# Performance work log

Measured on AMD Instinct MI355X. Metric: run time of the kernel, lower is better.

The kernel has to match this reference:

```python
import jax, jax.numpy as jnp
import numpy as np

N = 4096
D_IN = 3000
D_HID = 512
D_OUT = 64
NEG_SLOPE = 0.2  # LeakyReLU alpha used by GraphAttentionLayer(.., 0.2, 0.2)
MASK_FILL = -9e15


def setup_inputs() -> dict:
    key = jax.random.key(0)
    ks = jax.random.split(key, 13)

    def p(k, shape, fan_in):
        return jax.random.normal(k, shape, dtype=jnp.float32) * np.float32(1.0 / np.sqrt(fan_in))

    return {
        "features_omics1": jax.random.normal(ks[0], (N, D_IN), dtype=jnp.float32),
        "feat_adj_omics1": jax.random.randint(ks[1], (N, N), 0, 2, dtype=jnp.int32),
        "spatial_adj_omics1": jax.random.randint(ks[2], (N, N), 0, 2, dtype=jnp.int32),
        # encoder_1: GAT(D_IN -> D_HID); encoder_2: GAT(D_HID -> D_OUT)
        "W_enc1": p(ks[3], (D_IN, D_HID), D_IN),
        "a_enc1": p(ks[4], (2 * D_HID, 1), D_HID),
        "W_enc2": p(ks[5], (D_HID, D_OUT), D_HID),
        "a_enc2": p(ks[6], (2 * D_OUT, 1), D_OUT),
        # decoder_1: GAT(D_OUT -> D_HID); decoder_2: GAT(D_HID -> D_IN)
        "W_dec1": p(ks[7], (D_OUT, D_HID), D_OUT),
        "a_dec1": p(ks[8], (2 * D_HID, 1), D_HID),
        "W_dec2": p(ks[9], (D_HID, D_IN), D_HID),
        "a_dec2": p(ks[10], (2 * D_IN, 1), D_IN),
        # AttentionLayer fusion over the two views
        "w_omega": p(ks[11], (D_OUT, D_OUT), D_OUT),
        "u_omega": p(ks[12], (D_OUT, 1), D_OUT),
    }


def _gat(h, adj, W, a):
    """Canonical dense-adjacency GAT layer (pyGAT), dropout off, ELU output."""
    Wh = h @ W                                   # [N, F]
    f = W.shape[1]
    # e[i,j] = leaky_relu(a1.Wh_i + a2.Wh_j)
    e = jax.nn.leaky_relu(Wh @ a[:f] + (Wh @ a[f:]).T, NEG_SLOPE)  # [N, N]
    att = jax.nn.softmax(jnp.where(adj > 0, e, MASK_FILL), axis=1)
    return jax.nn.elu(att @ Wh)


def _encode(x, adj, W1, a1, W2, a2):
    return _gat(_gat(x, adj, W1, a1), adj, W2, a2)


def _att_fuse(e1, e2, w_omega, u_omega):
    emb = jnp.stack([e1, e2], axis=1)            # [N, 2, D]
    v = jnp.tanh(emb @ w_omega)                  # [N, 2, D]
    vu = (v @ u_omega)[..., 0]                   # [N, 2]
    alpha = jax.nn.softmax(vu + 1e-6, axis=1)    # [N, 2]
    fused = jnp.einsum('nkd,nk->nd', emb, alpha)
    return fused, alpha


def reference(features_omics1, feat_adj_omics1, spatial_adj_omics1,
              W_enc1, a_enc1, W_enc2, a_enc2,
              W_dec1, a_dec1, W_dec2, a_dec2,
              w_omega, u_omega):
    feat_emb = _encode(features_omics1, feat_adj_omics1, W_enc1, a_enc1, W_enc2, a_enc2)
    sp_emb = _encode(features_omics1, spatial_adj_omics1, W_enc1, a_enc1, W_enc2, a_enc2)
    emb_latent, alpha = _att_fuse(feat_emb, sp_emb, w_omega, u_omega)
    recon = _gat(_gat(emb_latent, spatial_adj_omics1, W_dec1, a_dec1),
                 spatial_adj_omics1, W_dec2, a_dec2)
    corr_f = _encode(recon, feat_adj_omics1, W_enc1, a_enc1, W_enc2, a_enc2)
    corr_s = _encode(recon, spatial_adj_omics1, W_enc1, a_enc1, W_enc2, a_enc2)
    corr, _ = _att_fuse(corr_f, corr_s, w_omega, u_omega)
    return emb_latent, recon, corr, alpha
```

## Files before the change

kernel.cpp:

```cpp
#include <hip/hip_runtime.h>
#include <hip/hip_bf16.h>
#include <math.h>

using u16 = unsigned short;
using u32 = unsigned int;

typedef __attribute__((ext_vector_type(8))) short s8v;
typedef __attribute__((ext_vector_type(4))) float f4v;

__device__ __forceinline__ float bf2f(u16 u) {
    u32 x = ((u32)u) << 16;
    return __builtin_bit_cast(float, x);
}
__device__ __forceinline__ u16 f2bf(float f) {
    u32 x = __builtin_bit_cast(u32, f);
    x += 0x7fffu + ((x >> 16) & 1u);
    return (u16)(x >> 16);
}

__device__ __forceinline__ f4v mfma_bf16(s8v a, s8v b, f4v c) {
    return __builtin_amdgcn_mfma_f32_16x16x32_bf16(a, b, c, 0, 0, 0);
}

#define GLL(srcp, dstp) __builtin_amdgcn_global_load_lds( \
    (const __attribute__((address_space(1))) void*)(srcp), \
    (__attribute__((address_space(3))) void*)(dstp), 16, 0, 0)

__device__ __forceinline__ void xcd_swz(int& bx, int& by, int& bz) {
    const int nx = gridDim.x, ny = gridDim.y;
    const int total = nx * ny * gridDim.z;
    int i = (bz * ny + by) * nx + bx;
    const int q = total >> 3, r = total & 7;
    const int xcd = i & 7, k = i >> 3;
    int j = ((xcd < r) ? xcd * (q + 1) : r * (q + 1) + (xcd - r) * q) + k;
    bx = j % nx; j /= nx;
    by = j % ny;
    bz = j / ny;
}

template<bool DO_ELU, bool OUT_F32>
__global__ __launch_bounds__(256) void tgemm(
    const u16* __restrict__ A, const u16* __restrict__ Bt,
    void* __restrict__ Cv, int M, int N, int K)
{
    constexpr int BM = 128, BN = 64, BK = 64;
    __shared__ __align__(16) u16 As[2][BM * BK];
    __shared__ __align__(16) u16 Bs[2][BN * BK];

    int bx = blockIdx.x, by = blockIdx.y, bz = blockIdx.z;
    xcd_swz(bx, by, bz);
    const int bm0 = by * BM, bn0 = bx * BN;
    const int tid = threadIdx.x;
    const int lane = tid & 63;
    const int wave = tid >> 6;
    const int wr = wave >> 1;
    const int wc = wave & 1;
    const int lr = lane & 15;
    const int srow = lane >> 3;
    const int schk = lane & 7;

    f4v acc[4][2] = {};

    auto stage = [&](int buf, int k0) {
#pragma unroll
        for (int ci = 0; ci < 4; ci++) {
            const int r8 = (wave * 4 + ci) * 8;
            const int row = r8 + srow;
            const int gchk = schk ^ (row & 7);
            GLL(A + (size_t)(bm0 + row) * K + k0 + gchk * 8, &As[buf][r8 * 64]);
        }
#pragma unroll
        for (int ci = 0; ci < 2; ci++) {
            const int r8 = (wave * 2 + ci) * 8;
            const int row = r8 + srow;
            int gn = bn0 + row;
            if (gn >= N) gn = N - 1;
            const int gchk = schk ^ (row & 7);
            GLL(Bt + (size_t)gn * K + k0 + gchk * 8, &Bs[buf][r8 * 64]);
        }
    };

    stage(0, 0);
    __syncthreads();
    int cur = 0;
    for (int k0 = 0; k0 < K; k0 += BK) {
        if (k0 + BK < K) stage(cur ^ 1, k0 + BK);
#pragma unroll
        for (int kk = 0; kk < 2; kk++) {
            const int cbase = (lane >> 4) + kk * 4;
            s8v a[4], b[2];
#pragma unroll
            for (int m = 0; m < 4; m++) {
                const int row = wr * 64 + m * 16 + lr;
                a[m] = *(const s8v*)&As[cur][row * 64 + (cbase ^ (row & 7)) * 8];
            }
#pragma unroll
            for (int n = 0; n < 2; n++) {
                const int row = wc * 32 + n * 16 + lr;
                b[n] = *(const s8v*)&Bs[cur][row * 64 + (cbase ^ (row & 7)) * 8];
            }
#pragma unroll
            for (int m = 0; m < 4; m++)
#pragma unroll
                for (int n = 0; n < 2; n++)
                    acc[m][n] = mfma_bf16(a[m], b[n], acc[m][n]);
        }
        __syncthreads();
        cur ^= 1;
    }

#pragma unroll
    for (int m = 0; m < 4; m++)
#pragma unroll
        for (int n = 0; n < 2; n++)
#pragma unroll
            for (int i = 0; i < 4; i++) {
                int gm = bm0 + wr * 64 + m * 16 + (lane >> 4) * 4 + i;
                int gn = bn0 + wc * 32 + n * 16 + lr;
                if (gm < M && gn < N) {
                    float val = acc[m][n][i];
                    if (DO_ELU) val = val > 0.f ? val : expm1f(val);
                    if (OUT_F32) ((float*)Cv)[(size_t)gm * N + gn] = val;
                    else         ((u16*)Cv)[(size_t)gm * N + gn] = f2bf(val);
                }
            }
}

__global__ __launch_bounds__(256) void tgemm_sk(
    const u16* __restrict__ A, const u16* __restrict__ Bt,
    float* __restrict__ P, int M, int N, int K, int KS)
{
    constexpr int BM = 128, BN = 64, BK = 64;
    __shared__ __align__(16) u16 As[2][BM * BK];
    __shared__ __align__(16) u16 Bs[2][BN * BK];

    int bx = blockIdx.x, by = blockIdx.y, kz = blockIdx.z;
    xcd_swz(bx, by, kz);
    const int bm0 = by * BM, bn0 = bx * BN;
    const int tid = threadIdx.x;
    const int lane = tid & 63;
    const int wave = tid >> 6;
    const int wr = wave >> 1;
    const int wc = wave & 1;
    const int lr = lane & 15;
    const int srow = lane >> 3;
    const int schk = lane & 7;

    f4v acc[4][2] = {};

    auto stage = [&](int buf, int k0) {
#pragma unroll
        for (int ci = 0; ci < 4; ci++) {
            const int r8 = (wave * 4 + ci) * 8;
            const int row = r8 + srow;
            const int gchk = schk ^ (row & 7);
            GLL(A + (size_t)(bm0 + row) * K + k0 + gchk * 8, &As[buf][r8 * 64]);
        }
#pragma unroll
        for (int ci = 0; ci < 2; ci++) {
            const int r8 = (wave * 2 + ci) * 8;
            const int row = r8 + srow;
            int gn = bn0 + row;
            if (gn >= N) gn = N - 1;
            const int gchk = schk ^ (row & 7);
            GLL(Bt + (size_t)gn * K + k0 + gchk * 8, &Bs[buf][r8 * 64]);
        }
    };

    const int kbeg = kz * KS, kend = kbeg + KS;
    stage(0, kbeg);
    __syncthreads();
    int cur = 0;
    for (int k0 = kbeg; k0 < kend; k0 += BK) {
        if (k0 + BK < kend) stage(cur ^ 1, k0 + BK);
#pragma unroll
        for (int kk = 0; kk < 2; kk++) {
            const int cbase = (lane >> 4) + kk * 4;
            s8v a[4], b[2];
#pragma unroll
            for (int m = 0; m < 4; m++) {
                const int row = wr * 64 + m * 16 + lr;
                a[m] = *(const s8v*)&As[cur][row * 64 + (cbase ^ (row & 7)) * 8];
            }
#pragma unroll
            for (int n = 0; n < 2; n++) {
                const int row = wc * 32 + n * 16 + lr;
                b[n] = *(const s8v*)&Bs[cur][row * 64 + (cbase ^ (row & 7)) * 8];
            }
#pragma unroll
            for (int m = 0; m < 4; m++)
#pragma unroll
                for (int n = 0; n < 2; n++)
                    acc[m][n] = mfma_bf16(a[m], b[n], acc[m][n]);
        }
        __syncthreads();
        cur ^= 1;
    }

    float* Pz = P + (size_t)kz * M * N;
#pragma unroll
    for (int m = 0; m < 4; m++)
#pragma unroll
        for (int n = 0; n < 2; n++)
#pragma unroll
            for (int i = 0; i < 4; i++) {
                int gm = bm0 + wr * 64 + m * 16 + (lane >> 4) * 4 + i;
                int gn = bn0 + wc * 32 + n * 16 + lr;
                if (gm < M && gn < N)
                    Pz[(size_t)gm * N + gn] = acc[m][n][i];
            }
}

template<bool ELU>
__global__ __launch_bounds__(256) void skred_kernel(
    const float* __restrict__ P, u16* __restrict__ out, int total, int sk)
{
    int i = blockIdx.x * 256 + threadIdx.x;
    if (i >= total) return;
    float s = 0.f;
    for (int z = 0; z < sk; z++) s += P[(size_t)z * total + i];
    if (ELU) s = s > 0.f ? s : expm1f(s);
    out[i] = f2bf(s);
}

template<bool ASP, bool SK>
__global__ __launch_bounds__(256) void tgemm2(
    const u16* __restrict__ A0, const u16* __restrict__ A1,
    const u16* __restrict__ Bt0, const u16* __restrict__ Bt1,
    void* __restrict__ Cv, int M, int N, int K, int KS)
{
    constexpr int BM = 128, BN = 64, BK = 64;
    __shared__ __align__(16) u16 As0[BM * BK];
    __shared__ __align__(16) u16 As1[ASP ? BM * BK : 8];
    __shared__ __align__(16) u16 Bs0[BN * BK];
    __shared__ __align__(16) u16 Bs1[BN * BK];

    int bx = blockIdx.x, by = blockIdx.y, kz = blockIdx.z;
    xcd_swz(bx, by, kz);
    const int bm0 = by * BM, bn0 = bx * BN;
    const int tid = threadIdx.x;
    const int lane = tid & 63;
    const int wave = tid >> 6;
    const int wr = wave >> 1;
    const int wc = wave & 1;
    const int lr = lane & 15;
    const int srow = lane >> 3;
    const int schk = lane & 7;

    f4v acc[4][2] = {};

    const int kbeg = SK ? kz * KS : 0;
    const int kend = SK ? kbeg + KS : K;
    for (int k0 = kbeg; k0 < kend; k0 += BK) {
#pragma unroll
        for (int ci = 0; ci < 4; ci++) {
            const int r8 = (wave * 4 + ci) * 8;
            const int row = r8 + srow;
            const int gchk = schk ^ (row & 7);
            const size_t goff = (size_t)(bm0 + row) * K + k0 + gchk * 8;
            GLL(A0 + goff, &As0[r8 * 64]);
            if constexpr (ASP) GLL(A1 + goff, &As1[r8 * 64]);
        }
#pragma unroll
        for (int ci = 0; ci < 2; ci++) {
            const int r8 = (wave * 2 + ci) * 8;
            const int row = r8 + srow;
            int gn = bn0 + row;
            if (gn >= N) gn = N - 1;
            const int gchk = schk ^ (row & 7);
            const size_t goff = (size_t)gn * K + k0 + gchk * 8;
            GLL(Bt0 + goff, &Bs0[r8 * 64]);
            GLL(Bt1 + goff, &Bs1[r8 * 64]);
        }
        __syncthreads();

#pragma unroll
        for (int kk = 0; kk < 2; kk++) {
            const int cbase = (lane >> 4) + kk * 4;
            s8v a0[4], a1[ASP ? 4 : 1], b0[2], b1[2];
#pragma unroll
            for (int m = 0; m < 4; m++) {
                const int row = wr * 64 + m * 16 + lr;
                const int o = row * 64 + (cbase ^ (row & 7)) * 8;
                a0[m] = *(const s8v*)&As0[o];
                if constexpr (ASP) a1[m] = *(const s8v*)&As1[o];
            }
#pragma unroll
            for (int n = 0; n < 2; n++) {
                const int row = wc * 32 + n * 16 + lr;
                const int o = row * 64 + (cbase ^ (row & 7)) * 8;
                b0[n] = *(const s8v*)&Bs0[o];
                b1[n] = *(const s8v*)&Bs1[o];
            }
#pragma unroll
            for (int m = 0; m < 4; m++)
#pragma unroll
                for (int n = 0; n < 2; n++) {
                    acc[m][n] = mfma_bf16(a0[m], b0[n], acc[m][n]);
                    acc[m][n] = mfma_bf16(a0[m], b1[n], acc[m][n]);
                    if constexpr (ASP) acc[m][n] = mfma_bf16(a1[m], b0[n], acc[m][n]);
                }
        }
        __syncthreads();
    }

#pragma unroll
    for (int m = 0; m < 4; m++)
#pragma unroll
        for (int n = 0; n < 2; n++)
#pragma unroll
            for (int i = 0; i < 4; i++) {
                int gm = bm0 + wr * 64 + m * 16 + (lane >> 4) * 4 + i;
                int gn = bn0 + wc * 32 + n * 16 + lr;
                if (gm < M && gn < N) {
                    if (SK) ((float*)Cv)[(size_t)kz * M * N + (size_t)gm * N + gn] = acc[m][n][i];
                    else    ((u16*)Cv)[(size_t)gm * N + gn] = f2bf(acc[m][n][i]);
                }
            }
}

__global__ __launch_bounds__(256) void splitA_kernel(
    const float* __restrict__ src, u16* __restrict__ hi, u16* __restrict__ lo,
    int C, int Cp)
{
    int r = blockIdx.y;
    int c = blockIdx.x * 256 + threadIdx.x;
    if (c >= Cp) return;
    float v = (c < C) ? src[(size_t)r * C + c] : 0.f;
    u16 h = f2bf(v);
    hi[(size_t)r * Cp + c] = h;
    lo[(size_t)r * Cp + c] = f2bf(v - bf2f(h));
}

__global__ __launch_bounds__(256) void splitBT_kernel(
    const float* __restrict__ src, u16* __restrict__ hi, u16* __restrict__ lo,
    int R, int C, int Rp)
{
    __shared__ float t[32][33];
    const int r0 = blockIdx.y * 32, c0 = blockIdx.x * 32;
    const int tr = threadIdx.x >> 5, tc = threadIdx.x & 31;
#pragma unroll
    for (int i = 0; i < 4; i++) {
        int r = r0 + tr + i * 8, c = c0 + tc;
        t[tr + i * 8][tc] = (r < R && c < C) ? src[(size_t)r * C + c] : 0.f;
    }
    __syncthreads();
#pragma unroll
    for (int i = 0; i < 4; i++) {
        int c = c0 + tr + i * 8, r = r0 + tc;
        if (c < C && r < Rp) {
            float v = t[tc][tr + i * 8];
            u16 h = f2bf(v);
            hi[(size_t)c * Rp + r] = h;
            lo[(size_t)c * Rp + r] = f2bf(v - bf2f(h));
        }
    }
}

__global__ __launch_bounds__(256) void tr_kernel(
    const u16* __restrict__ src, u16* __restrict__ dst, int R, int C)
{
    __shared__ u16 t[32][33];
    const int r0 = blockIdx.y * 32, c0 = blockIdx.x * 32;
    const int tr = threadIdx.x >> 5, tc = threadIdx.x & 31;
#pragma unroll
    for (int i = 0; i < 4; i++) {
        int r = r0 + tr + i * 8, c = c0 + tc;
        t[tr + i * 8][tc] = (r < R && c < C) ? src[(size_t)r * C + c] : (u16)0;
    }
    __syncthreads();
#pragma unroll
    for (int i = 0; i < 4; i++) {
        int c = c0 + tr + i * 8, r = r0 + tc;
        if (c < C && r < R) dst[(size_t)c * R + r] = t[tc][tr + i * 8];
    }
}

__device__ __forceinline__ float block_sum4(float v, float* red) {
#pragma unroll
    for (int off = 32; off; off >>= 1) v += __shfl_down(v, off);
    int w = threadIdx.x >> 6;
    if ((threadIdx.x & 63) == 0) red[w] = v;
    __syncthreads();
    float r = red[0] + red[1] + red[2] + red[3];
    __syncthreads();
    return r;
}
__device__ __forceinline__ float block_max4(float v, float* red) {
#pragma unroll
    for (int off = 32; off; off >>= 1) v = fmaxf(v, __shfl_down(v, off));
    int w = threadIdx.x >> 6;
    if ((threadIdx.x & 63) == 0) red[w] = v;
    __syncthreads();
    float r = fmaxf(fmaxf(red[0], red[1]), fmaxf(red[2], red[3]));
    __syncthreads();
    return r;
}

__global__ __launch_bounds__(256) void scores_kernel(
    const u16* __restrict__ Wh, int ld, int F, const float* __restrict__ a,
    float* __restrict__ s1, float* __restrict__ s2)
{
    __shared__ float red[4];
    int i = blockIdx.x, tid = threadIdx.x;
    float acc1 = 0.f, acc2 = 0.f;
    for (int f = tid; f < F; f += 256) {
        float w = bf2f(Wh[(size_t)i * ld + f]);
        acc1 += w * a[f];
        acc2 += w * a[F + f];
    }
    acc1 = block_sum4(acc1, red);
    acc2 = block_sum4(acc2, red);
    if (tid == 0) { s1[i] = acc1; s2[i] = acc2; }
}

__global__ __launch_bounds__(256) void att_kernel(
    const u32* __restrict__ mask, const float* __restrict__ s1,
    const float* __restrict__ s2, u16* __restrict__ att, int n)
{
    __shared__ float red[4];
    int i = blockIdx.x, tid = threadIdx.x;
    float s1i = s1[i];
    int j0 = tid * 16;
    u32 w = mask[(size_t)i * (n >> 5) + (j0 >> 5)];
    u32 bits = (j0 & 16) ? (w >> 16) : (w & 0xFFFFu);

    float e[16];
    float mx = -3.0e38f;
#pragma unroll
    for (int t = 0; t < 16; t++) {
        float x = s1i + s2[j0 + t];
        x = x > 0.f ? x : 0.2f * x;
        e[t] = x;
        if ((bits >> t) & 1u) mx = fmaxf(mx, x);
    }
    mx = block_max4(mx, red);

    float sum = 0.f;
#pragma unroll
    for (int t = 0; t < 16; t++) {
        float pv = ((bits >> t) & 1u) ? expf(e[t] - mx) : 0.f;
        e[t] = pv;
        sum += pv;
    }
    sum = block_sum4(sum, red);
    float rinv = sum > 0.f ? 1.f / sum : 0.f;
#pragma unroll
    for (int t = 0; t < 16; t++)
        att[(size_t)i * n + j0 + t] = f2bf(e[t] * rinv);
}

__global__ __launch_bounds__(64) void fuse_kernel(
    const u16* __restrict__ E1, const u16* __restrict__ E2,
    const float* __restrict__ W, const float* __restrict__ U,
    float* __restrict__ fused, float* __restrict__ alpha)
{
    __shared__ float e1[64], e2[64];
    int i = blockIdx.x, d = threadIdx.x;
    e1[d] = bf2f(E1[i * 64 + d]);
    e2[d] = bf2f(E2[i * 64 + d]);
    __syncthreads();
    float v1 = 0.f, v2 = 0.f;
#pragma unroll 8
    for (int f = 0; f < 64; f++) {
        float w = W[f * 64 + d];
        v1 += e1[f] * w;
        v2 += e2[f] * w;
    }
    v1 = tanhf(v1); v2 = tanhf(v2);
    float u = U[d];
    float p1 = v1 * u, p2 = v2 * u;
#pragma unroll
    for (int off = 32; off; off >>= 1) {
        p1 += __shfl_down(p1, off);
        p2 += __shfl_down(p2, off);
    }
    p1 = __shfl(p1, 0); p2 = __shfl(p2, 0);
    float m = fmaxf(p1, p2);
    float w1 = expf(p1 - m), w2 = expf(p2 - m);
    float a1 = w1 / (w1 + w2), a2 = w2 / (w1 + w2);
    fused[i * 64 + d] = a1 * e1[d] + a2 * e2[d];
    if (alpha != nullptr && d < 2) alpha[i * 2 + d] = (d == 0 ? a1 : a2);
}

__global__ void bitpack_kernel(const int* __restrict__ adj,
                               u32* __restrict__ mask, int nwords)
{
    int w = blockIdx.x * 256 + threadIdx.x;
    if (w >= nwords) return;
    const int* src = adj + (size_t)w * 32;
    u32 m = 0;
#pragma unroll
    for (int b = 0; b < 32; b++) m |= (src[b] > 0 ? 1u : 0u) << b;
    mask[w] = m;
}

extern "C" void kernel_launch(void* const* d_in, const int* in_sizes, int n_in,
                              void* d_out, int out_size, void* d_ws, size_t ws_size,
                              hipStream_t stream)
{
    const int N = 4096, DIN = 3000, DINP = 3008, DH = 512, DO = 64;
    const float* x      = (const float*)d_in[0];
    const int*   adjF   = (const int*)d_in[1];
    const int*   adjS   = (const int*)d_in[2];
    const float* We1    = (const float*)d_in[3];
    const float* aE1    = (const float*)d_in[4];
    const float* We2    = (const float*)d_in[5];
    const float* aE2    = (const float*)d_in[6];
    const float* Wd1    = (const float*)d_in[7];
    const float* aD1    = (const float*)d_in[8];
    const float* Wd2    = (const float*)d_in[9];
    const float* aD2    = (const float*)d_in[10];
    const float* Womega = (const float*)d_in[11];
    const float* Uomega = (const float*)d_in[12];

    float* out       = (float*)d_out;
    float* out_emb   = out;
    float* out_recon = out + (size_t)N * DO;
    float* out_corr  = out_recon + (size_t)N * DIN;
    float* out_alpha = out_corr + (size_t)N * DO;

    char* ws = (char*)d_ws;
    size_t off = 0;
    auto alloc = [&](size_t bytes) {
        size_t o = off; off += (bytes + 255) & ~(size_t)255; return o;
    };
    const size_t o_att   = alloc((size_t)2 * N * N * 2);
    const size_t o_maskF = alloc((size_t)N * (N / 32) * 4);
    const size_t o_maskS = alloc((size_t)N * (N / 32) * 4);
    const size_t o_s1    = alloc((size_t)N * 4);
    const size_t o_s2    = alloc((size_t)N * 4);
    const size_t o_wh1   = alloc((size_t)N * DH * 2);
    const size_t o_h1    = alloc((size_t)2 * N * DH * 2);
    const size_t o_whd1  = alloc((size_t)N * DH * 2);
    const size_t o_d1    = alloc((size_t)N * DH * 2);
    const size_t o_whd2  = alloc((size_t)N * DIN * 2);
    size_t o_b64[8];
    for (int i = 0; i < 8; i++) o_b64[i] = alloc((size_t)N * DO * 2);
    const size_t o_t512  = alloc((size_t)DH * N * 2);
    const size_t o_td1   = alloc((size_t)DH * N * 2);
    const size_t o_td2   = alloc((size_t)DIN * N * 2);
    const size_t o_t64a  = alloc((size_t)DO * N * 2);
    const size_t o_t64b  = alloc((size_t)DO * N * 2);
    const size_t o_xh    = alloc((size_t)N * DINP * 2);
    const size_t o_xl    = alloc((size_t)N * DINP * 2);
    const size_t o_we1th = alloc((size_t)DH * DINP * 2);
    const size_t o_we1tl = alloc((size_t)DH * DINP * 2);
    const size_t o_we2th = alloc((size_t)DO * DH * 2);
    const size_t o_we2tl = alloc((size_t)DO * DH * 2);
    const size_t o_wd1th = alloc((size_t)DH * DO * 2);
    const size_t o_wd1tl = alloc((size_t)DH * DO * 2);
    const size_t o_wd2th = alloc((size_t)DIN * DH * 2);
    const size_t o_wd2tl = alloc((size_t)DIN * DH * 2);
    const size_t o_eh    = alloc((size_t)N * DO * 2);
    const size_t o_el    = alloc((size_t)N * DO * 2);
    const size_t o_skp   = alloc((size_t)8 * N * DO * 4);

    u16* attF   = (u16*)(ws + o_att);
    u16* attS   = attF + (size_t)N * N;
    u32* maskF  = (u32*)(ws + o_maskF);
    u32* maskS  = (u32*)(ws + o_maskS);
    float* s1   = (float*)(ws + o_s1);
    float* s2   = (float*)(ws + o_s2);
    u16* wh1x   = (u16*)(ws + o_wh1);
    u16* whc1   = (u16*)(ws + o_wh1);
    u16* h1     = (u16*)(ws + o_h1);
    u16* h1f    = h1;
    u16* h1s    = h1 + (size_t)N * DH;
    u16* c1f    = h1f;
    u16* c1s    = h1s;
    u16* whd1   = (u16*)(ws + o_whd1);
    u16* d1b    = (u16*)(ws + o_d1);
    u16* whd2   = (u16*)(ws + o_whd2);
    u16* wh2f   = (u16*)(ws + o_b64[0]);
    u16* wh2s   = (u16*)(ws + o_b64[1]);
    u16* h2f    = (u16*)(ws + o_b64[2]);
    u16* h2s    = (u16*)(ws + o_b64[3]);
    u16* whc2f  = (u16*)(ws + o_b64[4]);
    u16* whc2s  = (u16*)(ws + o_b64[5]);
    u16* c2f    = (u16*)(ws + o_b64[6]);
    u16* c2s    = (u16*)(ws + o_b64[7]);
    u16* t512   = (u16*)(ws + o_t512);
    u16* td1    = (u16*)(ws + o_td1);
    u16* td2    = (u16*)(ws + o_td2);
    u16* t64a   = (u16*)(ws + o_t64a);
    u16* t64b   = (u16*)(ws + o_t64b);
    u16* xh     = (u16*)(ws + o_xh);
    u16* xl     = (u16*)(ws + o_xl);
    u16* we1th  = (u16*)(ws + o_we1th);
    u16* we1tl  = (u16*)(ws + o_we1tl);
    u16* we2th  = (u16*)(ws + o_we2th);
    u16* we2tl  = (u16*)(ws + o_we2tl);
    u16* wd1th  = (u16*)(ws + o_wd1th);
    u16* wd1tl  = (u16*)(ws + o_wd1tl);
    u16* wd2th  = (u16*)(ws + o_wd2th);
    u16* wd2tl  = (u16*)(ws + o_wd2tl);
    u16* eh     = (u16*)(ws + o_eh);
    u16* el     = (u16*)(ws + o_el);
    float* skp  = (float*)(ws + o_skp);

    auto grid = [](int M, int Nn) { return dim3((Nn + 63) / 64, (M + 127) / 128); };
    auto gatt = [&](const u16* A, const u16* Bt, u16* C, int M, int Nn) {
        tgemm<true, false><<<grid(M, Nn), 256, 0, stream>>>(A, Bt, C, M, Nn, N);
    };
    auto gatt_f32 = [&](const u16* A, const u16* Bt, float* C, int Nn) {
        tgemm<true, true><<<grid(N, Nn), 256, 0, stream>>>(A, Bt, C, N, Nn, N);
    };
    auto gatt_sk = [&](const u16* A, const u16* Bt, u16* C) {
        tgemm_sk<<<dim3(1, 32, 8), 256, 0, stream>>>(A, Bt, skp, N, DO, N, 512);
        skred_kernel<true><<<(N * DO + 255) / 256, 256, 0, stream>>>(skp, C, N * DO, 8);
    };
    auto wgemm_s = [&](const u16* A0, const u16* A1, const u16* Bt0, const u16* Bt1,
                       u16* C, int Nn, int K) {
        tgemm2<true, false><<<grid(N, Nn), 256, 0, stream>>>(A0, A1, Bt0, Bt1, C, N, Nn, K, K);
    };
    auto wgemm_h = [&](const u16* A0, const u16* Bt0, const u16* Bt1,
                       u16* C, int Nn, int K) {
        tgemm2<false, false><<<grid(N, Nn), 256, 0, stream>>>(A0, nullptr, Bt0, Bt1, C, N, Nn, K, K);
    };
    auto wgemm64_sk = [&](const u16* A0, const u16* Bt0, const u16* Bt1, u16* C) {
        tgemm2<false, true><<<dim3(1, 32, 8), 256, 0, stream>>>(
            A0, nullptr, Bt0, Bt1, skp, N, DO, DH, 64);
        skred_kernel<false><<<(N * DO + 255) / 256, 256, 0, stream>>>(skp, C, N * DO, 8);
    };
    auto splitA = [&](const float* src, u16* hi, u16* lo, int C, int Cp) {
        splitA_kernel<<<dim3((Cp + 255) / 256, N), 256, 0, stream>>>(src, hi, lo, C, Cp);
    };
    auto splitBT = [&](const float* src, u16* hi, u16* lo, int R, int C, int Rp) {
        splitBT_kernel<<<dim3((C + 31) / 32, (Rp + 31) / 32), 256, 0, stream>>>(src, hi, lo, R, C, Rp);
    };
    auto tr = [&](const u16* src, u16* dst, int R, int C) {
        tr_kernel<<<dim3((C + 31) / 32, (R + 31) / 32), 256, 0, stream>>>(src, dst, R, C);
    };
    auto scores = [&](const u16* Wh, int ld, int F, const float* a) {
        scores_kernel<<<N, 256, 0, stream>>>(Wh, ld, F, a, s1, s2);
    };
    auto attb = [&](const u32* mask, u16* dst) {
        att_kernel<<<N, 256, 0, stream>>>(mask, s1, s2, dst, N);
    };

    bitpack_kernel<<<(N * (N / 32) + 255) / 256, 256, 0, stream>>>(adjF, maskF, N * (N / 32));
    bitpack_kernel<<<(N * (N / 32) + 255) / 256, 256, 0, stream>>>(adjS, maskS, N * (N / 32));
    splitA(x, xh, xl, DIN, DINP);
    splitBT(We1, we1th, we1tl, DIN, DH, DINP);
    splitBT(We2, we2th, we2tl, DH, DO, DH);
    splitBT(Wd1, wd1th, wd1tl, DO, DH, DO);
    splitBT(Wd2, wd2th, wd2tl, DH, DIN, DH);

    wgemm_s(xh, xl, we1th, we1tl, wh1x, DH, DINP);
    tr(wh1x, t512, N, DH);
    scores(wh1x, DH, DH, aE1);
    attb(maskF, attF);
    attb(maskS, attS);
    gatt(attF, t512, h1, 2 * N, DH);

    wgemm64_sk(h1f, we2th, we2tl, wh2f);
    tr(wh2f, t64a, N, DO);
    scores(wh2f, DO, DO, aE2);
    attb(maskF, attF); gatt_sk(attF, t64a, h2f);
    wgemm64_sk(h1s, we2th, we2tl, wh2s);
    tr(wh2s, t64b, N, DO);
    scores(wh2s, DO, DO, aE2);
    attb(maskS, attS); gatt_sk(attS, t64b, h2s);

    fuse_kernel<<<N, 64, 0, stream>>>(h2f, h2s, Womega, Uomega, out_emb, out_alpha);

    splitA(out_emb, eh, el, DO, DO);
    wgemm_s(eh, el, wd1th, wd1tl, whd1, DH, DO);
    tr(whd1, td1, N, DH);
    scores(whd1, DH, DH, aD1);
    attb(maskS, attS); gatt(attS, td1, d1b, N, DH);

    wgemm_h(d1b, wd2th, wd2tl, whd2, DIN, DH);
    tr(whd2, td2, N, DIN);
    scores(whd2, DIN, DIN, aD2);
    attb(maskS, attS); gatt_f32(attS, td2, out_recon, DIN);

    splitA(out_recon, xh, xl, DIN, DINP);
    wgemm_s(xh, xl, we1th, we1tl, whc1, DH, DINP);
    tr(whc1, t512, N, DH);
    scores(whc1, DH, DH, aE1);
    attb(maskF, attF);
    attb(maskS, attS);
    gatt(attF, t512, h1, 2 * N, DH);

    wgemm64_sk(c1f, we2th, we2tl, whc2f);
    tr(whc2f, t64a, N, DO);
    scores(whc2f, DO, DO, aE2);
    attb(maskF, attF); gatt_sk(attF, t64a, c2f);
    wgemm64_sk(c1s, we2th, we2tl, whc2s);
    tr(whc2s, t64b, N, DO);
    scores(whc2s, DO, DO, aE2);
    attb(maskS, attS); gatt_sk(attS, t64b, c2s);

    fuse_kernel<<<N, 64, 0, stream>>>(c2f, c2s, Womega, Uomega, out_corr, nullptr);
}
```

Measured before the change: 1.087 ms.

## Batch both views of layer 2, fuse split/score/transpose epilogues, double-buffer tgemm2

Runs the second encoder layer for both adjacency views in one pass. This uses stacked-row GEMMs, a split-K reduce kernel that also computes attention scores and the transposed copies, a dual-mask attention kernel, and a split-K aggregation that picks its B matrix per row half. The hi/lo bf16 split of recon and of the fused embedding moves into the epilogues of the producing kernels, so the separate splitA launches are dropped. tgemm2 is changed to BK=32 with double-buffered LDS prefetch. The aim is fewer launches, fewer memory round trips and better overlap of loads with MFMA. The cost is more code and larger workspace buffers.

```diff
diff --git a/kernel.cpp b/kernel.cpp
--- a/kernel.cpp
+++ b/kernel.cpp
@@ -38,10 +38,11 @@
     bz = j / ny;
 }
 
-template<bool DO_ELU, bool OUT_F32>
+template<bool DO_ELU, bool OUT_F32, bool OUT_SPLIT>
 __global__ __launch_bounds__(256) void tgemm(
     const u16* __restrict__ A, const u16* __restrict__ Bt,
-    void* __restrict__ Cv, int M, int N, int K)
+    void* __restrict__ Cv, int M, int N, int K,
+    u16* __restrict__ Sh, u16* __restrict__ Sl, int Cp)
 {
     constexpr int BM = 128, BN = 64, BK = 64;
     __shared__ __align__(16) u16 As[2][BM * BK];
@@ -53,11 +54,9 @@
     const int tid = threadIdx.x;
     const int lane = tid & 63;
     const int wave = tid >> 6;
-    const int wr = wave >> 1;
-    const int wc = wave & 1;
+    const int wr = wave >> 1, wc = wave & 1;
     const int lr = lane & 15;
-    const int srow = lane >> 3;
-    const int schk = lane & 7;
+    const int srow = lane >> 3, schk = lane & 7;
 
     f4v acc[4][2] = {};
 
@@ -120,15 +119,24 @@
                 if (gm < M && gn < N) {
                     float val = acc[m][n][i];
                     if (DO_ELU) val = val > 0.f ? val : expm1f(val);
-                    if (OUT_F32) ((float*)Cv)[(size_t)gm * N + gn] = val;
-                    else         ((u16*)Cv)[(size_t)gm * N + gn] = f2bf(val);
+                    if (OUT_F32) {
+                        ((float*)Cv)[(size_t)gm * N + gn] = val;
+                        if (OUT_SPLIT) {
+                            u16 hv = f2bf(val);
+                            Sh[(size_t)gm * Cp + gn] = hv;
+                            Sl[(size_t)gm * Cp + gn] = f2bf(val - bf2f(hv));
+                        }
+                    } else {
+                        ((u16*)Cv)[(size_t)gm * N + gn] = f2bf(val);
+                    }
                 }
             }
 }
 
-__global__ __launch_bounds__(256) void tgemm_sk(
-    const u16* __restrict__ A, const u16* __restrict__ Bt,
-    float* __restrict__ P, int M, int N, int K, int KS)
+__global__ __launch_bounds__(256) void tgemm_skd(
+    const u16* __restrict__ A, const u16* __restrict__ BtA,
+    const u16* __restrict__ BtB, float* __restrict__ P,
+    int M, int Mh, int N, int K, int KS)
 {
     constexpr int BM = 128, BN = 64, BK = 64;
     __shared__ __align__(16) u16 As[2][BM * BK];
@@ -137,14 +145,13 @@
     int bx = blockIdx.x, by = blockIdx.y, kz = blockIdx.z;
     xcd_swz(bx, by, kz);
     const int bm0 = by * BM, bn0 = bx * BN;
+    const u16* Bt = (bm0 < Mh) ? BtA : BtB;
     const int tid = threadIdx.x;
     const int lane = tid & 63;
     const int wave = tid >> 6;
-    const int wr = wave >> 1;
-    const int wc = wave & 1;
+    const int wr = wave >> 1, wc = wave & 1;
     const int lr = lane & 15;
-    const int srow = lane >> 3;
-    const int schk = lane & 7;
+    const int srow = lane >> 3, schk = lane & 7;
 
     f4v acc[4][2] = {};
 
@@ -229,11 +236,11 @@
     const u16* __restrict__ Bt0, const u16* __restrict__ Bt1,
     void* __restrict__ Cv, int M, int N, int K, int KS)
 {
-    constexpr int BM = 128, BN = 64, BK = 64;
-    __shared__ __align__(16) u16 As0[BM * BK];
-    __shared__ __align__(16) u16 As1[ASP ? BM * BK : 8];
-    __shared__ __align__(16) u16 Bs0[BN * BK];
-    __shared__ __align__(16) u16 Bs1[BN * BK];
+    constexpr int BM = 128, BN = 64, BK = 32;
+    __shared__ __align__(16) u16 As0[2][BM * BK];
+    __shared__ __align__(16) u16 As1[ASP ? 2 : 1][ASP ? BM * BK : 8];
+    __shared__ __align__(16) u16 Bs0[2][BN * BK];
+    __shared__ __align__(16) u16 Bs1[2][BN * BK];
 
     int bx = blockIdx.x, by = blockIdx.y, kz = blockIdx.z;
     xcd_swz(bx, by, kz);
@@ -241,56 +248,60 @@
     const int tid = threadIdx.x;
     const int lane = tid & 63;
     const int wave = tid >> 6;
-    const int wr = wave >> 1;
-    const int wc = wave & 1;
+    const int wr = wave >> 1, wc = wave & 1;
     const int lr = lane & 15;
-    const int srow = lane >> 3;
-    const int schk = lane & 7;
+    const int srow = lane >> 2;
+    const int schk = lane & 3;
+
+    auto swzr = [](int row) { return (row & 3) ^ ((row >> 2) & 1); };
 
     f4v acc[4][2] = {};
+
+    auto stage = [&](int buf, int k0) {
+#pragma unroll
+        for (int ci = 0; ci < 2; ci++) {
+            const int r16 = (wave * 2 + ci) * 16;
+            const int row = r16 + srow;
+            const int gchk = schk ^ swzr(row);
+            const size_t goff = (size_t)(bm0 + row) * K + k0 + gchk * 8;
+            GLL(A0 + goff, &As0[buf][r16 * 32]);
+            if constexpr (ASP) GLL(A1 + goff, &As1[buf][r16 * 32]);
+        }
+        {
+            const int r16 = wave * 16;
+            const int row = r16 + srow;
+            int gn = bn0 + row;
+            if (gn >= N) gn = N - 1;
+            const int gchk = schk ^ swzr(row);
+            const size_t goff = (size_t)gn * K + k0 + gchk * 8;
+            GLL(Bt0 + goff, &Bs0[buf][r16 * 32]);
+            GLL(Bt1 + goff, &Bs1[buf][r16 * 32]);
+        }
+    };
 
     const int kbeg = SK ? kz * KS : 0;
     const int kend = SK ? kbeg + KS : K;
+    stage(0, kbeg);
+    __syncthreads();
+    int cur = 0;
     for (int k0 = kbeg; k0 < kend; k0 += BK) {
-#pragma unroll
-        for (int ci = 0; ci < 4; ci++) {
-            const int r8 = (wave * 4 + ci) * 8;
-            const int row = r8 + srow;
-            const int gchk = schk ^ (row & 7);
-            const size_t goff = (size_t)(bm0 + row) * K + k0 + gchk * 8;
-            GLL(A0 + goff, &As0[r8 * 64]);
-            if constexpr (ASP) GLL(A1 + goff, &As1[r8 * 64]);
-        }
-#pragma unroll
-        for (int ci = 0; ci < 2; ci++) {
-            const int r8 = (wave * 2 + ci) * 8;
-            const int row = r8 + srow;
-            int gn = bn0 + row;
-            if (gn >= N) gn = N - 1;
-            const int gchk = schk ^ (row & 7);
-            const size_t goff = (size_t)gn * K + k0 + gchk * 8;
-            GLL(Bt0 + goff, &Bs0[r8 * 64]);
-            GLL(Bt1 + goff, &Bs1[r8 * 64]);
-        }
-        __syncthreads();
-
-#pragma unroll
-        for (int kk = 0; kk < 2; kk++) {
-            const int cbase = (lane >> 4) + kk * 4;
+        if (k0 + BK < kend) stage(cur ^ 1, k0 + BK);
+        {
+            const int cbase = lane >> 4;
             s8v a0[4], a1[ASP ? 4 : 1], b0[2], b1[2];
 #pragma unroll
             for (int m = 0; m < 4; m++) {
                 const int row = wr * 64 + m * 16 + lr;
-                const int o = row * 64 + (cbase ^ (row & 7)) * 8;
-                a0[m] = *(const s8v*)&As0[o];
-                if constexpr (ASP) a1[m] = *(const s8v*)&As1[o];
+                const int o = row * 32 + (cbase ^ swzr(row)) * 8;
+                a0[m] = *(const s8v*)&As0[cur][o];
+                if constexpr (ASP) a1[m] = *(const s8v*)&As1[cur][o];
             }
 #pragma unroll
             for (int n = 0; n < 2; n++) {
                 const int row = wc * 32 + n * 16 + lr;
-                const int o = row * 64 + (cbase ^ (row & 7)) * 8;
-                b0[n] = *(const s8v*)&Bs0[o];
-                b1[n] = *(const s8v*)&Bs1[o];
+                const int o = row * 32 + (cbase ^ swzr(row)) * 8;
+                b0[n] = *(const s8v*)&Bs0[cur][o];
+                b1[n] = *(const s8v*)&Bs1[cur][o];
             }
 #pragma unroll
             for (int m = 0; m < 4; m++)
@@ -302,6 +313,7 @@
                 }
         }
         __syncthreads();
+        cur ^= 1;
     }
 
 #pragma unroll
@@ -319,6 +331,60 @@
             }
 }
 
+__global__ __launch_bounds__(256) void skredTS_kernel(
+    const float* __restrict__ P, const float* __restrict__ a,
+    u16* __restrict__ wh, u16* __restrict__ tA, u16* __restrict__ tB,
+    float* __restrict__ s1, float* __restrict__ s2, int n, int sk)
+{
+    __shared__ u16 lds[64][72];
+    const int rowbase = blockIdx.x * 64;
+    const int t = threadIdx.x;
+    const int rl = t >> 2, cg = t & 3;
+    const int row = rowbase + rl;
+    const size_t M2 = (size_t)2 * n;
+
+    float v[16];
+#pragma unroll
+    for (int k = 0; k < 16; k++) v[k] = 0.f;
+    for (int z = 0; z < sk; z++) {
+        const float4* p = (const float4*)&P[((size_t)z * M2 + row) * 64 + cg * 16];
+#pragma unroll
+        for (int q = 0; q < 4; q++) {
+            float4 x = p[q];
+            v[q * 4 + 0] += x.x; v[q * 4 + 1] += x.y;
+            v[q * 4 + 2] += x.z; v[q * 4 + 3] += x.w;
+        }
+    }
+    u16 w[16];
+    float p1 = 0.f, p2 = 0.f;
+#pragma unroll
+    for (int k = 0; k < 16; k++) {
+        w[k] = f2bf(v[k]);
+        float vr = bf2f(w[k]);
+        int f = cg * 16 + k;
+        p1 += vr * a[f];
+        p2 += vr * a[64 + f];
+    }
+    *(s8v*)&wh[(size_t)row * 64 + cg * 16]     = *(s8v*)&w[0];
+    *(s8v*)&wh[(size_t)row * 64 + cg * 16 + 8] = *(s8v*)&w[8];
+    *(s8v*)&lds[rl][cg * 16]     = *(s8v*)&w[0];
+    *(s8v*)&lds[rl][cg * 16 + 8] = *(s8v*)&w[8];
+
+    p1 += __shfl_down(p1, 1); p1 += __shfl_down(p1, 2);
+    p2 += __shfl_down(p2, 1); p2 += __shfl_down(p2, 2);
+    if (cg == 0) { s1[row] = p1; s2[row] = p2; }
+    __syncthreads();
+
+    const bool hb = rowbase >= n;
+    u16* tX = hb ? tB : tA;
+    const int grow = rowbase - (hb ? n : 0);
+    u16 o[16];
+#pragma unroll
+    for (int k = 0; k < 16; k++) o[k] = lds[cg * 16 + k][rl];
+    *(s8v*)&tX[(size_t)rl * n + grow + cg * 16]     = *(s8v*)&o[0];
+    *(s8v*)&tX[(size_t)rl * n + grow + cg * 16 + 8] = *(s8v*)&o[8];
+}
+
 __global__ __launch_bounds__(256) void splitA_kernel(
     const float* __restrict__ src, u16* __restrict__ hi, u16* __restrict__ lo,
     int C, int Cp)
@@ -414,13 +480,12 @@
     if (tid == 0) { s1[i] = acc1; s2[i] = acc2; }
 }
 
-__global__ __launch_bounds__(256) void att_kernel(
-    const u32* __restrict__ mask, const float* __restrict__ s1,
-    const float* __restrict__ s2, u16* __restrict__ att, int n)
-{
-    __shared__ float red[4];
-    int i = blockIdx.x, tid = threadIdx.x;
-    float s1i = s1[i];
+__device__ __forceinline__ void att_row(
+    const u32* mask, const float* s1, const float* s2, int soff,
+    u16* att, int i, int n, float* red)
+{
+    int tid = threadIdx.x;
+    float s1i = s1[soff + i];
     int j0 = tid * 16;
     u32 w = mask[(size_t)i * (n >> 5) + (j0 >> 5)];
     u32 bits = (j0 & 16) ? (w >> 16) : (w & 0xFFFFu);
@@ -429,7 +494,7 @@
     float mx = -3.0e38f;
 #pragma unroll
     for (int t = 0; t < 16; t++) {
-        float x = s1i + s2[j0 + t];
+        float x = s1i + s2[soff + j0 + t];
         x = x > 0.f ? x : 0.2f * x;
         e[t] = x;
         if ((bits >> t) & 1u) mx = fmaxf(mx, x);
@@ -450,10 +515,30 @@
         att[(size_t)i * n + j0 + t] = f2bf(e[t] * rinv);
 }
 
+__global__ __launch_bounds__(256) void att_kernel(
+    const u32* __restrict__ mask, const float* __restrict__ s1,
+    const float* __restrict__ s2, u16* __restrict__ att, int n)
+{
+    __shared__ float red[4];
+    att_row(mask, s1, s2, 0, att, blockIdx.x, n, red);
+}
+
+__global__ __launch_bounds__(256) void att2_kernel(
+    const u32* __restrict__ maskA, const u32* __restrict__ maskB,
+    const float* __restrict__ s1, const float* __restrict__ s2, int offB,
+    u16* __restrict__ attA, u16* __restrict__ attB, int n)
+{
+    __shared__ float red[4];
+    int b = blockIdx.x;
+    if (b < n) att_row(maskA, s1, s2, 0, attA, b, n, red);
+    else      att_row(maskB, s1, s2, offB, attB, b - n, n, red);
+}
+
 __global__ __launch_bounds__(64) void fuse_kernel(
     const u16* __restrict__ E1, const u16* __restrict__ E2,
     const float* __restrict__ W, const float* __restrict__ U,
-    float* __restrict__ fused, float* __restrict__ alpha)
+    float* __restrict__ fused, float* __restrict__ alpha,
+    u16* __restrict__ eh, u16* __restrict__ el)
 {
     __shared__ float e1[64], e2[64];
     int i = blockIdx.x, d = threadIdx.x;
@@ -479,7 +564,13 @@
     float m = fmaxf(p1, p2);
     float w1 = expf(p1 - m), w2 = expf(p2 - m);
     float a1 = w1 / (w1 + w2), a2 = w2 / (w1 + w2);
-    fused[i * 64 + d] = a1 * e1[d] + a2 * e2[d];
+    float fv = a1 * e1[d] + a2 * e2[d];
+    fused[i * 64 + d] = fv;
+    if (eh != nullptr) {
+        u16 hv = f2bf(fv);
+        eh[i * 64 + d] = hv;
+        el[i * 64 + d] = f2bf(fv - bf2f(hv));
+    }
     if (alpha != nullptr && d < 2) alpha[i * 2 + d] = (d == 0 ? a1 : a2);
 }
 
@@ -528,15 +619,15 @@
     const size_t o_att   = alloc((size_t)2 * N * N * 2);
     const size_t o_maskF = alloc((size_t)N * (N / 32) * 4);
     const size_t o_maskS = alloc((size_t)N * (N / 32) * 4);
-    const size_t o_s1    = alloc((size_t)N * 4);
-    const size_t o_s2    = alloc((size_t)N * 4);
+    const size_t o_s1    = alloc((size_t)2 * N * 4);
+    const size_t o_s2    = alloc((size_t)2 * N * 4);
     const size_t o_wh1   = alloc((size_t)N * DH * 2);
     const size_t o_h1    = alloc((size_t)2 * N * DH * 2);
     const size_t o_whd1  = alloc((size_t)N * DH * 2);
     const size_t o_d1    = alloc((size_t)N * DH * 2);
     const size_t o_whd2  = alloc((size_t)N * DIN * 2);
-    size_t o_b64[8];
-    for (int i = 0; i < 8; i++) o_b64[i] = alloc((size_t)N * DO * 2);
+    const size_t o_wh2   = alloc((size_t)2 * N * DO * 2);
+    const size_t o_h2    = alloc((size_t)2 * N * DO * 2);
     const size_t o_t512  = alloc((size_t)DH * N * 2);
     const size_t o_td1   = alloc((size_t)DH * N * 2);
     const size_t o_td2   = alloc((size_t)DIN * N * 2);
@@ -554,7 +645,7 @@
     const size_t o_wd2tl = alloc((size_t)DIN * DH * 2);
     const size_t o_eh    = alloc((size_t)N * DO * 2);
     const size_t o_el    = alloc((size_t)N * DO * 2);
-    const size_t o_skp   = alloc((size_t)8 * N * DO * 4);
+    const size_t o_skp   = alloc((size_t)8 * 2 * N * DO * 4);
 
     u16* attF   = (u16*)(ws + o_att);
     u16* attS   = attF + (size_t)N * N;
@@ -565,21 +656,13 @@
     u16* wh1x   = (u16*)(ws + o_wh1);
     u16* whc1   = (u16*)(ws + o_wh1);
     u16* h1     = (u16*)(ws + o_h1);
-    u16* h1f    = h1;
-    u16* h1s    = h1 + (size_t)N * DH;
-    u16* c1f    = h1f;
-    u16* c1s    = h1s;
     u16* whd1   = (u16*)(ws + o_whd1);
     u16* d1b    = (u16*)(ws + o_d1);
     u16* whd2   = (u16*)(ws + o_whd2);
-    u16* wh2f   = (u16*)(ws + o_b64[0]);
-    u16* wh2s   = (u16*)(ws + o_b64[1]);
-    u16* h2f    = (u16*)(ws + o_b64[2]);
-    u16* h2s    = (u16*)(ws + o_b64[3]);
-    u16* whc2f  = (u16*)(ws + o_b64[4]);
-    u16* whc2s  = (u16*)(ws + o_b64[5]);
-    u16* c2f    = (u16*)(ws + o_b64[6]);
-    u16* c2s    = (u16*)(ws + o_b64[7]);
+    u16* wh2    = (u16*)(ws + o_wh2);
+    u16* h2     = (u16*)(ws + o_h2);
+    u16* h2f    = h2;
+    u16* h2s    = h2 + (size_t)N * DO;
     u16* t512   = (u16*)(ws + o_t512);
     u16* td1    = (u16*)(ws + o_td1);
     u16* td2    = (u16*)(ws + o_td2);
@@ -601,33 +684,8 @@
 
     auto grid = [](int M, int Nn) { return dim3((Nn + 63) / 64, (M + 127) / 128); };
     auto gatt = [&](const u16* A, const u16* Bt, u16* C, int M, int Nn) {
-        tgemm<true, false><<<grid(M, Nn), 256, 0, stream>>>(A, Bt, C, M, Nn, N);
-    };
-    auto gatt_f32 = [&](const u16* A, const u16* Bt, float* C, int Nn) {
-        tgemm<true, true><<<grid(N, Nn), 256, 0, stream>>>(A, Bt, C, N, Nn, N);
-    };
-    auto gatt_sk = [&](const u16* A, const u16* Bt, u16* C) {
-        tgemm_sk<<<dim3(1, 32, 8), 256, 0, stream>>>(A, Bt, skp, N, DO, N, 512);
-        skred_kernel<true><<<(N * DO + 255) / 256, 256, 0, stream>>>(skp, C, N * DO, 8);
-    };
-    auto wgemm_s = [&](const u16* A0, const u16* A1, const u16* Bt0, const u16* Bt1,
-                       u16* C, int Nn, int K) {
-        tgemm2<true, false><<<grid(N, Nn), 256, 0, stream>>>(A0, A1, Bt0, Bt1, C, N, Nn, K, K);
-    };
-    auto wgemm_h = [&](const u16* A0, const u16* Bt0, const u16* Bt1,
-                       u16* C, int Nn, int K) {
-        tgemm2<false, false><<<grid(N, Nn), 256, 0, stream>>>(A0, nullptr, Bt0, Bt1, C, N, Nn, K, K);
-    };
-    auto wgemm64_sk = [&](const u16* A0, const u16* Bt0, const u16* Bt1, u16* C) {
-        tgemm2<false, true><<<dim3(1, 32, 8), 256, 0, stream>>>(
-            A0, nullptr, Bt0, Bt1, skp, N, DO, DH, 64);
-        skred_kernel<false><<<(N * DO + 255) / 256, 256, 0, stream>>>(skp, C, N * DO, 8);
-    };
-    auto splitA = [&](const float* src, u16* hi, u16* lo, int C, int Cp) {
-        splitA_kernel<<<dim3((Cp + 255) / 256, N), 256, 0, stream>>>(src, hi, lo, C, Cp);
-    };
-    auto splitBT = [&](const float* src, u16* hi, u16* lo, int R, int C, int Rp) {
-        splitBT_kernel<<<dim3((C + 31) / 32, (Rp + 31) / 32), 256, 0, stream>>>(src, hi, lo, R, C, Rp);
+        tgemm<true, false, false><<<grid(M, Nn), 256, 0, stream>>>(
+            A, Bt, C, M, Nn, N, nullptr, nullptr, 0);
     };
     auto tr = [&](const u16* src, u16* dst, int R, int C) {
         tr_kernel<<<dim3((C + 31) / 32, (R + 31) / 32), 256, 0, stream>>>(src, dst, R, C);
@@ -635,63 +693,61 @@
     auto scores = [&](const u16* Wh, int ld, int F, const float* a) {
         scores_kernel<<<N, 256, 0, stream>>>(Wh, ld, F, a, s1, s2);
     };
-    auto attb = [&](const u32* mask, u16* dst) {
-        att_kernel<<<N, 256, 0, stream>>>(mask, s1, s2, dst, N);
+    auto layer2 = [&](const u16* Astacked, u16* wh2buf, u16* h2out) {
+        tgemm2<false, true><<<dim3(1, 64, 8), 256, 0, stream>>>(
+            Astacked, nullptr, we2th, we2tl, skp, 2 * N, DO, DH, 64);
+        skredTS_kernel<<<2 * N / 64, 256, 0, stream>>>(
+            skp, aE2, wh2buf, t64a, t64b, s1, s2, N, 8);
+        att2_kernel<<<2 * N, 256, 0, stream>>>(
+            maskF, maskS, s1, s2, N, attF, attS, N);
+        tgemm_skd<<<dim3(1, 64, 8), 256, 0, stream>>>(
+            attF, t64a, t64b, skp, 2 * N, N, DO, N, 512);
+        skred_kernel<true><<<(2 * N * DO + 255) / 256, 256, 0, stream>>>(
+            skp, h2out, 2 * N * DO, 8);
     };
 
     bitpack_kernel<<<(N * (N / 32) + 255) / 256, 256, 0, stream>>>(adjF, maskF, N * (N / 32));
     bitpack_kernel<<<(N * (N / 32) + 255) / 256, 256, 0, stream>>>(adjS, maskS, N * (N / 32));
-    splitA(x, xh, xl, DIN, DINP);
-    splitBT(We1, we1th, we1tl, DIN, DH, DINP);
-    splitBT(We2, we2th, we2tl, DH, DO, DH);
-    splitBT(Wd1, wd1th, wd1tl, DO, DH, DO);
-    splitBT(Wd2, wd2th, wd2tl, DH, DIN, DH);
-
-    wgemm_s(xh, xl, we1th, we1tl, wh1x, DH, DINP);
+    splitA_kernel<<<dim3((DINP + 255) / 256, N), 256, 0, stream>>>(x, xh, xl, DIN, DINP);
+    splitBT_kernel<<<dim3((DH + 31) / 32, (DINP + 31) / 32), 256, 0, stream>>>(We1, we1th, we1tl, DIN, DH, DINP);
+    splitBT_kernel<<<dim3((DO + 31) / 32, (DH + 31) / 32), 256, 0, stream>>>(We2, we2th, we2tl, DH, DO, DH);
+    splitBT_kernel<<<dim3((DH + 31) / 32, (DO + 31) / 32), 256, 0, stream>>>(Wd1, wd1th, wd1tl, DO, DH, DO);
+    splitBT_kernel<<<dim3((DIN + 31) / 32, (DH + 31) / 32), 256, 0, stream>>>(Wd2, wd2th, wd2tl, DH, DIN, DH);
+
+    tgemm2<true, false><<<grid(N, DH), 256, 0, stream>>>(
+        xh, xl, we1th, we1tl, wh1x, N, DH, DINP, DINP);
     tr(wh1x, t512, N, DH);
     scores(wh1x, DH, DH, aE1);
-    attb(maskF, attF);
-    attb(maskS, attS);
+    att2_kernel<<<2 * N, 256, 0, stream>>>(maskF, maskS, s1, s2, 0, attF, attS, N);
     gatt(attF, t512, h1, 2 * N, DH);
 
-    wgemm64_sk(h1f, we2th, we2tl, wh2f);
-    tr(wh2f, t64a, N, DO);
-    scores(wh2f, DO, DO, aE2);
-    attb(maskF, attF); gatt_sk(attF, t64a, h2f);
-    wgemm64_sk(h1s, we2th, we2tl, wh2s);
-    tr(wh2s, t64b, N, DO);
-    scores(wh2s, DO, DO, aE2);
-    attb(maskS, attS); gatt_sk(attS, t64b, h2s);
-
-    fuse_kernel<<<N, 64, 0, stream>>>(h2f, h2s, Womega, Uomega, out_emb, out_alpha);
-
-    splitA(out_emb, eh, el, DO, DO);
-    wgemm_s(eh, el, wd1th, wd1tl, whd1, DH, DO);
+    layer2(h1, wh2, h2);
+
+    fuse_kernel<<<N, 64, 0, stream>>>(h2f, h2s, Womega, Uomega, out_emb, out_alpha, eh, el);
+
+    tgemm2<true, false><<<grid(N, DH), 256, 0, stream>>>(
+        eh, el, wd1th, wd1tl, whd1, N, DH, DO, DO);
     tr(whd1, td1, N, DH);
     scores(whd1, DH, DH, aD1);
-    attb(maskS, attS); gatt(attS, td1, d1b, N, DH);
-
-    wgemm_h(d1b, wd2th, wd2tl, whd2, DIN, DH);
+    att_kernel<<<N, 256, 0, stream>>>(maskS, s1, s2, attS, N);
+    gatt(attS, td1, d1b, N, DH);
+
+    tgemm2<false, false><<<grid(N, DIN), 256, 0, stream>>>(
+        d1b, nullptr, wd2th, wd2tl, whd2, N, DIN, DH, DH);
     tr(whd2, td2, N, DIN);
     scores(whd2, DIN, DIN, aD2);
-    attb(maskS, attS); gatt_f32(attS, td2, out_recon, DIN);
-
-    splitA(out_recon, xh, xl, DIN, DINP);
-    wgemm_s(xh, xl, we1th, we1tl, whc1, DH, DINP);
+    att_kernel<<<N, 256, 0, stream>>>(maskS, s1, s2, attS, N);
+    tgemm<true, true, true><<<grid(N, DIN), 256, 0, stream>>>(
+        attS, td2, out_recon, N, DIN, N, xh, xl, DINP);
+
+    tgemm2<true, false><<<grid(N, DH), 256, 0, stream>>>(
+        xh, xl, we1th, we1tl, whc1, N, DH, DINP, DINP);
     tr(whc1, t512, N, DH);
     scores(whc1, DH, DH, aE1);
-    attb(maskF, attF);
-    attb(maskS, attS);
+    att2_kernel<<<2 * N, 256, 0, stream>>>(maskF, maskS, s1, s2, 0, attF, attS, N);
     gatt(attF, t512, h1, 2 * N, DH);
 
-    wgemm64_sk(c1f, we2th, we2tl, whc2f);
-    tr(whc2f, t64a, N, DO);
-    scores(whc2f, DO, DO, aE2);
-    attb(maskF, attF); gatt_sk(attF, t64a, c2f);
-    wgemm64_sk(c1s, we2th, we2tl, whc2s);
-    tr(whc2s, t64b, N, DO);
-    scores(whc2s, DO, DO, aE2);
-    attb(maskS, attS); gatt_sk(attS, t64b, c2s);
-
-    fuse_kernel<<<N, 64, 0, stream>>>(c2f, c2s, Womega, Uomega, out_corr, nullptr);
-}
+    layer2(h1, wh2, h2);
+
+    fuse_kernel<<<N, 64, 0, stream>>>(h2f, h2s, Womega, Uomega, out_corr, nullptr, nullptr, nullptr);
+}
```

Result: faster. 993.0 us (-8.7%).
